# Kernel optimization log

Measured on AMD Instinct MI355X. Metric: run time of the kernel, lower is better.

Reference implementation:

```python
import jax, jax.numpy as jnp
import numpy as np
from jax import lax

T, B = 256, 4096
H = 64  # lstm hidden/input size


def setup_inputs() -> dict:
    key = jax.random.key(0)
    ks = jax.random.split(key, 20)
    s = 0.1
    return {
        "x": jax.random.normal(ks[0], (T * B, 9), jnp.float32),
        "done": jax.random.randint(ks[1], (T * B,), 0, 2).astype(jnp.int32),
        "h0": jax.random.normal(ks[2], (1, B, H), jnp.float32),
        "c0": jax.random.normal(ks[3], (1, B, H), jnp.float32),
        # root MLP: Linear(9,32) ReLU Linear(32,64) ReLU (stored [in,out])
        "Wr1": jax.random.normal(ks[4], (9, 32), jnp.float32) * s,
        "br1": jnp.zeros((32,), jnp.float32),
        "Wr2": jax.random.normal(ks[5], (32, H), jnp.float32) * s,
        "br2": jnp.zeros((H,), jnp.float32),
        # LSTM(64,64): gate order i,f,g,o; stored [in, 4H]
        "Wih": jax.random.normal(ks[6], (H, 4 * H), jnp.float32) * s,
        "Whh": jax.random.normal(ks[7], (H, 4 * H), jnp.float32) * s,
        "b_lstm": jnp.zeros((4 * H,), jnp.float32),  # bias_ih + bias_hh (both init 0)
        # critic: Linear(64,16) Tanh Linear(16,8) Tanh Linear(8,1)
        "Wc1": jax.random.normal(ks[8], (H, 16), jnp.float32) * s,
        "bc1": jnp.zeros((16,), jnp.float32),
        "Wc2": jax.random.normal(ks[9], (16, 8), jnp.float32) * s,
        "bc2": jnp.zeros((8,), jnp.float32),
        "Wc3": jax.random.normal(ks[10], (8, 1), jnp.float32) * s,
        "bc3": jnp.zeros((1,), jnp.float32),
    }


def reference(x, done, h0, c0, Wr1, br1, Wr2, br2, Wih, Whh, b_lstm,
              Wc1, bc1, Wc2, bc2, Wc3, bc3):
    b = h0.shape[1]
    # root MLP on all T*B rows at once
    hidden = jax.nn.relu(jax.nn.relu(x @ Wr1 + br1) @ Wr2 + br2)  # [T*B, 64]
    t = hidden.shape[0] // b
    hid = hidden.reshape(t, b, H)
    d = done.reshape(t, b).astype(hidden.dtype)
    # precompute input projection for all timesteps (hoisted out of the scan)
    xp = hid @ Wih + b_lstm  # [T, B, 4H]

    def step(carry, inp):
        h, c = carry
        xpt, dt = inp
        m = (1.0 - dt)[:, None]  # reset state where episode is done
        h = h * m
        c = c * m
        g = xpt + h @ Whh  # [B, 4H]
        gi, gf, gg, go = jnp.split(g, 4, axis=-1)
        c = jax.nn.sigmoid(gf) * c + jax.nn.sigmoid(gi) * jnp.tanh(gg)
        h = jax.nn.sigmoid(go) * jnp.tanh(c)
        return (h, c), h

    (_, _), hs = lax.scan(step, (h0[0], c0[0]), (xp, d))
    new_hidden = hs.reshape(t * b, H)  # flatten like torch.cat + flatten(0,1)
    # critic head (get_value)
    v = jnp.tanh(new_hidden @ Wc1 + bc1)
    v = jnp.tanh(v @ Wc2 + bc2)
    return v @ Wc3 + bc3  # [T*B, 1]
```

## Files before the change

kernel.cpp:

```cpp
#include <hip/hip_runtime.h>
#include <hip/hip_bf16.h>


#define TT 256
#define BB 4096
#define TBROWS (TT * BB)
#define LOG2E 1.44269504088896340736f

typedef short bf16x8 __attribute__((ext_vector_type(8)));
typedef float f32x4 __attribute__((ext_vector_type(4)));

__device__ __forceinline__ unsigned bfbits(float x) {
  unsigned u = __float_as_uint(x);
  return (u + 0x7fffu + ((u >> 16) & 1u)) >> 16;
}
__device__ __forceinline__ unsigned pkbf(float lo, float hi) {
  return bfbits(lo) | (bfbits(hi) << 16);
}
__device__ __forceinline__ unsigned short cvt1bf(float x) {
  unsigned pk;
  asm("v_cvt_pk_bf16_f32 %0, %1, %2" : "=v"(pk) : "v"(x), "v"(x));
  return (unsigned short)pk;
}
__device__ __forceinline__ float rcpf_(float x) { return __builtin_amdgcn_rcpf(x); }
__device__ __forceinline__ float exp2f_(float x) { return __builtin_amdgcn_exp2f(x); }

#define BAR_LDS()                                                   \
  do {                                                              \
    asm volatile("s_waitcnt lgkmcnt(0)" ::: "memory");              \
    __builtin_amdgcn_s_barrier();                                   \
    asm volatile("" ::: "memory");                                  \
  } while (0)

__global__ __launch_bounds__(256) void k1m(const float* __restrict__ x,
                                           const float* __restrict__ Wr1,
                                           const float* __restrict__ br1,
                                           const float* __restrict__ Wr2,
                                           const float* __restrict__ br2,
                                           unsigned short* __restrict__ hb) {
  __shared__ int sBr1[2 * 256];
  __shared__ int sBr2[4 * 256];
  __shared__ float sx[4][208];
  __shared__ int h1s[4][324];

  const int tid = threadIdx.x;
  const int lane = tid & 63, wid = tid >> 6;
  const int g4 = lane >> 4, l15 = lane & 15;

  for (int i = tid; i < 512; i += 256) {
    int nt = i >> 8, rem = i & 255;
    int L = rem >> 2, d = rem & 3;
    int u = nt * 16 + (L & 15);
    int k0 = (L >> 4) * 4 + d;
    float v0 = (k0 < 9) ? Wr1[k0 * 32 + u] : 0.f;
    sBr1[i] = (int)bfbits(v0);
  }
  for (int i = tid; i < 1024; i += 256) {
    int nt = i >> 8, rem = i & 255;
    int L = rem >> 2, d = rem & 3;
    int u = nt * 16 + (L & 15);
    int p = (L >> 4) * 4 + d;
    sBr2[i] = (int)pkbf(Wr2[p * 64 + u], Wr2[(p + 16) * 64 + u]);
  }
  __syncthreads();

  float br1v[2] = {br1[l15], br1[16 + l15]};
  float br2v[4];
#pragma unroll
  for (int nt = 0; nt < 4; ++nt) br2v[nt] = br2[nt * 16 + l15];

  long gw = (long)blockIdx.x * 4 + wid;
  long nw = (long)gridDim.x * 4;
  for (long row0 = gw * 16; row0 < TBROWS; row0 += nw * 16) {
    {
      int j = lane;
      float v = x[row0 * 9 + j];
      int r = (j * 456) >> 12; int cc = j - r * 9;
      sx[wid][r * 12 + cc] = v;
      j = lane + 64;
      v = x[row0 * 9 + j];
      r = (j * 456) >> 12; cc = j - r * 9;
      sx[wid][r * 12 + cc] = v;
      if (lane < 16) {
        j = lane + 128;
        v = x[row0 * 9 + j];
        r = (j * 456) >> 12; cc = j - r * 9;
        sx[wid][r * 12 + cc] = v;
      }
    }
    float4 xq = *(const float4*)&sx[wid][l15 * 12 + g4 * 4];
    union { unsigned u[4]; bf16x8 v; } A1;
#pragma unroll
    for (int d = 0; d < 4; ++d) {
      float v = ((const float*)&xq)[d];
      v = (g4 * 4 + d < 9) ? v : 0.f;
      A1.u[d] = bfbits(v);
    }
    f32x4 c1[2];
#pragma unroll
    for (int nt = 0; nt < 2; ++nt) {
      c1[nt] = (f32x4){br1v[nt], br1v[nt], br1v[nt], br1v[nt]};
      c1[nt] = __builtin_amdgcn_mfma_f32_16x16x32_bf16(
          A1.v, *(const bf16x8*)&sBr1[nt * 256 + lane * 4], c1[nt], 0, 0, 0);
    }
#pragma unroll
    for (int r = 0; r < 4; ++r)
      h1s[wid][(g4 * 4 + r) * 20 + l15] =
          (int)pkbf(fmaxf(c1[0][r], 0.f), fmaxf(c1[1][r], 0.f));
    bf16x8 A2 = *(const bf16x8*)&h1s[wid][l15 * 20 + g4 * 4];
    f32x4 c2[4];
#pragma unroll
    for (int nt = 0; nt < 4; ++nt) {
      c2[nt] = (f32x4){br2v[nt], br2v[nt], br2v[nt], br2v[nt]};
      c2[nt] = __builtin_amdgcn_mfma_f32_16x16x32_bf16(
          A2, *(const bf16x8*)&sBr2[nt * 256 + lane * 4], c2[nt], 0, 0, 0);
    }
#pragma unroll
    for (int nt = 0; nt < 4; ++nt)
#pragma unroll
      for (int r = 0; r < 4; ++r)
        hb[(row0 + g4 * 4 + r) * 64 + nt * 16 + l15] =
            (unsigned short)bfbits(fmaxf(c2[nt][r], 0.f));
  }
}

__global__ __launch_bounds__(320) void k2m(
    const unsigned short* __restrict__ hb, const int* __restrict__ done,
    const float* __restrict__ h0, const float* __restrict__ c0,
    const float* __restrict__ Wih, const float* __restrict__ Whh,
    const float* __restrict__ bl,
    const float* __restrict__ Wc1, const float* __restrict__ bc1,
    const float* __restrict__ Wc2, const float* __restrict__ bc2,
    const float* __restrict__ Wc3, const float* __restrict__ bc3,
    float* __restrict__ out) {
  __shared__ __align__(16) unsigned short hT2[2][16 * 72];
  __shared__ float sv1[16 * 20];
  __shared__ __align__(16) float smask[TT * 16];
  __shared__ int sdn[TT * 16];

  const int tid = threadIdx.x;
  const int lane = tid & 63;
  const int wid = tid >> 6;
  const int g4 = lane >> 4, l15 = lane & 15;
  const int base_b = blockIdx.x * 16;

  for (int i = tid; i < TT * 16; i += 320) {
    int d = done[(long)(i >> 4) * BB + base_b + (i & 15)];
    sdn[i] = d;
    smask[i] = 1.f - (float)d;
  }

  union frag { unsigned u[4]; bf16x8 v; };
  frag Bih[4][2], Bhh[4][2];
  frag Bc1[2];
  float wc2a[16], wc2b[16];
  float c[4];
  f32x4 bias_acc[4];
  float bc1s = 0.f, bc2s0 = 0.f, bc2s1 = 0.f, wc3a = 0.f, wc3b = 0.f, bc3r = 0.f;

  if (wid < 4) {
#pragma unroll
    for (int g = 0; g < 4; ++g) {
      int nt = g * 4 + wid;
      int col = nt * 16 + l15;
      float sc = (g == 2) ? 2.f * LOG2E : LOG2E;
#pragma unroll
      for (int q = 0; q < 2; ++q)
#pragma unroll
        for (int d = 0; d < 4; ++d) {
          int k0 = q * 32 + g4 * 8 + 2 * d;
          Bih[g][q].u[d] = pkbf(Wih[k0 * 256 + col] * sc, Wih[(k0 + 1) * 256 + col] * sc);
          Bhh[g][q].u[d] = pkbf(Whh[k0 * 256 + col] * sc, Whh[(k0 + 1) * 256 + col] * sc);
        }
      float bv = bl[nt * 16 + l15] * sc;
      bias_acc[g] = (f32x4){bv, bv, bv, bv};
    }
#pragma unroll
    for (int r = 0; r < 4; ++r) {
      int row = base_b + g4 * 4 + r;
      float m0 = 1.f - (float)done[row];
      c[r] = c0[row * 64 + wid * 16 + l15] * m0;
      hT2[1][(g4 * 4 + r) * 72 + wid * 16 + l15] =
          (unsigned short)bfbits(h0[row * 64 + wid * 16 + l15]);
    }
  } else {
    float S = 2.f * LOG2E;
#pragma unroll
    for (int q = 0; q < 2; ++q)
#pragma unroll
      for (int d = 0; d < 4; ++d) {
        int k0 = q * 32 + g4 * 8 + 2 * d;
        Bc1[q].u[d] = pkbf(Wc1[k0 * 16 + l15] * S, Wc1[(k0 + 1) * 16 + l15] * S);
      }
#pragma unroll
    for (int k = 0; k < 16; ++k) {
      wc2a[k] = Wc2[k * 8 + g4 * 2] * S;
      wc2b[k] = Wc2[k * 8 + g4 * 2 + 1] * S;
    }
    bc1s = bc1[l15] * S;
    bc2s0 = bc2[g4 * 2] * S;
    bc2s1 = bc2[g4 * 2 + 1] * S;
    wc3a = Wc3[g4 * 2];
    wc3b = Wc3[g4 * 2 + 1];
    bc3r = bc3[0];
  }
  __syncthreads();

  bf16x8 aA0 = {}, aA1 = {}, aB0 = {}, aB1 = {};
  int dnA = 0, dnB = 0;
  if (wid < 4) {
    long r0a = ((long)0 * BB + base_b + l15) * 64;
    long r1a = ((long)1 * BB + base_b + l15) * 64;
    aA0 = *(const bf16x8*)(hb + r0a + g4 * 8);
    aA1 = *(const bf16x8*)(hb + r0a + 32 + g4 * 8);
    aB0 = *(const bf16x8*)(hb + r1a + g4 * 8);
    aB1 = *(const bf16x8*)(hb + r1a + 32 + g4 * 8);
    dnA = sdn[0 * 16 + l15];
    dnB = sdn[1 * 16 + l15];
  }

  auto gate_step = [&](int t, bf16x8& x0, bf16x8& x1, int& dnv) {
    const unsigned short* rb = hT2[(t + 1) & 1];
    unsigned short* wb = hT2[t & 1];
    __builtin_amdgcn_s_setprio(1);
    int4 r0 = *(const int4*)(rb + l15 * 72 + g4 * 8);
    int4 r1 = *(const int4*)(rb + l15 * 72 + 32 + g4 * 8);
    int tm = (t + 1 < TT) ? t + 1 : t;
    float4 mn4 = *(const float4*)&smask[tm * 16 + g4 * 4];
    f32x4 acc[4];
#pragma unroll
    for (int g = 0; g < 4; ++g)
      acc[g] = __builtin_amdgcn_mfma_f32_16x16x32_bf16(x0, Bih[g][0].v, bias_acc[g], 0, 0, 0);
#pragma unroll
    for (int g = 0; g < 4; ++g)
      acc[g] = __builtin_amdgcn_mfma_f32_16x16x32_bf16(x1, Bih[g][1].v, acc[g], 0, 0, 0);
    if (dnv != 0) { r0 = make_int4(0, 0, 0, 0); r1 = make_int4(0, 0, 0, 0); }
    union { int4 i4; bf16x8 v; } ah0, ah1;
    ah0.i4 = r0; ah1.i4 = r1;
#pragma unroll
    for (int g = 0; g < 4; ++g)
      acc[g] = __builtin_amdgcn_mfma_f32_16x16x32_bf16(ah0.v, Bhh[g][0].v, acc[g], 0, 0, 0);
#pragma unroll
    for (int g = 0; g < 4; ++g)
      acc[g] = __builtin_amdgcn_mfma_f32_16x16x32_bf16(ah1.v, Bhh[g][1].v, acc[g], 0, 0, 0);
    if (t + 2 < TT) {
      long nb = ((long)(t + 2) * BB + base_b + l15) * 64;
      x0 = *(const bf16x8*)(hb + nb + g4 * 8);
      x1 = *(const bf16x8*)(hb + nb + 32 + g4 * 8);
      dnv = sdn[(t + 2) * 16 + l15];
    }
#pragma unroll
    for (int r = 0; r < 4; ++r) {
      float xi = acc[0][r], xf = acc[1][r], xg = acc[2][r], xo = acc[3][r];
      float si = rcpf_(1.f + exp2f_(-xi));
      float sf = rcpf_(1.f + exp2f_(-xf));
      float so = rcpf_(1.f + exp2f_(-xo));
      float tg = fmaf(2.f, rcpf_(1.f + exp2f_(-xg)), -1.f);
      float cc = fmaf(sf, c[r], si * tg);
      float tc = fmaf(2.f, rcpf_(1.f + exp2f_(cc * (-2.f * LOG2E))), -1.f);
      float oh = so * tc;
      c[r] = cc * ((const float*)&mn4)[r];
      wb[(g4 * 4 + r) * 72 + wid * 16 + l15] = cvt1bf(oh);
    }
    __builtin_amdgcn_s_setprio(0);
  };

  auto critic_step = [&](int tprev, const unsigned short* rb) {
    bf16x8 ca0 = *(const bf16x8*)(rb + l15 * 72 + g4 * 8);
    bf16x8 ca1 = *(const bf16x8*)(rb + l15 * 72 + 32 + g4 * 8);
    f32x4 a1 = (f32x4){bc1s, bc1s, bc1s, bc1s};
    a1 = __builtin_amdgcn_mfma_f32_16x16x32_bf16(ca0, Bc1[0].v, a1, 0, 0, 0);
    a1 = __builtin_amdgcn_mfma_f32_16x16x32_bf16(ca1, Bc1[1].v, a1, 0, 0, 0);
#pragma unroll
    for (int r = 0; r < 4; ++r) {
      float v1 = fmaf(2.f, rcpf_(1.f + exp2f_(-a1[r])), -1.f);
      sv1[(g4 * 4 + r) * 20 + l15] = v1;
    }
    float a2a = bc2s0, a2b = bc2s1;
    const float* vrow = &sv1[l15 * 20];
#pragma unroll
    for (int k = 0; k < 16; ++k) {
      float vk = vrow[k];
      a2a = fmaf(vk, wc2a[k], a2a);
      a2b = fmaf(vk, wc2b[k], a2b);
    }
    float v2a = fmaf(2.f, rcpf_(1.f + exp2f_(-a2a)), -1.f);
    float v2b = fmaf(2.f, rcpf_(1.f + exp2f_(-a2b)), -1.f);
    float p = fmaf(v2a, wc3a, v2b * wc3b);
    p += __shfl_xor(p, 16);
    p += __shfl_xor(p, 32);
    if (g4 == 0) out[(long)tprev * BB + base_b + l15] = p + bc3r;
  };

  for (int t2 = 0; t2 < TT; t2 += 2) {
    if (wid < 4) {
      gate_step(t2, aA0, aA1, dnA);
    } else {
      if (t2 > 0) critic_step(t2 - 1, hT2[(t2 + 1) & 1]);
    }
    BAR_LDS();
    if (wid < 4) {
      gate_step(t2 + 1, aB0, aB1, dnB);
    } else {
      critic_step(t2, hT2[(t2 + 2) & 1]);
    }
    BAR_LDS();
  }
  if (wid == 4) critic_step(TT - 1, hT2[(TT - 1) & 1]);
}

extern "C" void kernel_launch(void* const* d_in, const int* in_sizes, int n_in,
                              void* d_out, int out_size, void* d_ws, size_t ws_size,
                              hipStream_t stream) {
  const float* x = (const float*)d_in[0];
  const int* done = (const int*)d_in[1];
  const float* h0 = (const float*)d_in[2];
  const float* c0 = (const float*)d_in[3];
  const float* Wr1 = (const float*)d_in[4];
  const float* br1 = (const float*)d_in[5];
  const float* Wr2 = (const float*)d_in[6];
  const float* br2 = (const float*)d_in[7];
  const float* Wih = (const float*)d_in[8];
  const float* Whh = (const float*)d_in[9];
  const float* bl = (const float*)d_in[10];
  const float* Wc1 = (const float*)d_in[11];
  const float* bc1 = (const float*)d_in[12];
  const float* Wc2 = (const float*)d_in[13];
  const float* bc2 = (const float*)d_in[14];
  const float* Wc3 = (const float*)d_in[15];
  const float* bc3 = (const float*)d_in[16];
  float* out = (float*)d_out;

  unsigned short* hb = (unsigned short*)d_ws;

  k1m<<<dim3(1024), dim3(256), 0, stream>>>(x, Wr1, br1, Wr2, br2, hb);
  k2m<<<dim3(256), dim3(320), 0, stream>>>(hb, done, h0, c0, Wih, Whh, bl,
                                           Wc1, bc1, Wc2, bc2, Wc3, bc3, out);
}
```

Measured before the change: 197.5 us.

## Precompute next step's input projection off the recurrent critical path

```diff
diff --git a/kernel.cpp b/kernel.cpp
--- a/kernel.cpp
+++ b/kernel.cpp
@@ -206,20 +206,29 @@
   }
   __syncthreads();
 
+  f32x4 accP[4], accQ[4];
   bf16x8 aA0 = {}, aA1 = {}, aB0 = {}, aB1 = {};
   int dnA = 0, dnB = 0;
   if (wid < 4) {
-    long r0a = ((long)0 * BB + base_b + l15) * 64;
+    long rx = ((long)base_b + l15) * 64;
+    bf16x8 x00 = *(const bf16x8*)(hb + rx + g4 * 8);
+    bf16x8 x01 = *(const bf16x8*)(hb + rx + 32 + g4 * 8);
+#pragma unroll
+    for (int g = 0; g < 4; ++g) {
+      accP[g] = __builtin_amdgcn_mfma_f32_16x16x32_bf16(x00, Bih[g][0].v, bias_acc[g], 0, 0, 0);
+      accP[g] = __builtin_amdgcn_mfma_f32_16x16x32_bf16(x01, Bih[g][1].v, accP[g], 0, 0, 0);
+    }
     long r1a = ((long)1 * BB + base_b + l15) * 64;
-    aA0 = *(const bf16x8*)(hb + r0a + g4 * 8);
-    aA1 = *(const bf16x8*)(hb + r0a + 32 + g4 * 8);
-    aB0 = *(const bf16x8*)(hb + r1a + g4 * 8);
-    aB1 = *(const bf16x8*)(hb + r1a + 32 + g4 * 8);
+    long r2a = ((long)2 * BB + base_b + l15) * 64;
+    aA0 = *(const bf16x8*)(hb + r1a + g4 * 8);
+    aA1 = *(const bf16x8*)(hb + r1a + 32 + g4 * 8);
+    aB0 = *(const bf16x8*)(hb + r2a + g4 * 8);
+    aB1 = *(const bf16x8*)(hb + r2a + 32 + g4 * 8);
     dnA = sdn[0 * 16 + l15];
     dnB = sdn[1 * 16 + l15];
   }
 
-  auto gate_step = [&](int t, bf16x8& x0, bf16x8& x1, int& dnv) {
+  auto gate_step = [&](int t, f32x4* accW, f32x4* accN, bf16x8& x0, bf16x8& x1, int& dnv) {
     const unsigned short* rb = hT2[(t + 1) & 1];
     unsigned short* wb = hT2[t & 1];
     __builtin_amdgcn_s_setprio(1);
@@ -227,28 +236,30 @@
     int4 r1 = *(const int4*)(rb + l15 * 72 + 32 + g4 * 8);
     int tm = (t + 1 < TT) ? t + 1 : t;
     float4 mn4 = *(const float4*)&smask[tm * 16 + g4 * 4];
-    f32x4 acc[4];
-#pragma unroll
-    for (int g = 0; g < 4; ++g)
-      acc[g] = __builtin_amdgcn_mfma_f32_16x16x32_bf16(x0, Bih[g][0].v, bias_acc[g], 0, 0, 0);
-#pragma unroll
-    for (int g = 0; g < 4; ++g)
-      acc[g] = __builtin_amdgcn_mfma_f32_16x16x32_bf16(x1, Bih[g][1].v, acc[g], 0, 0, 0);
     if (dnv != 0) { r0 = make_int4(0, 0, 0, 0); r1 = make_int4(0, 0, 0, 0); }
     union { int4 i4; bf16x8 v; } ah0, ah1;
     ah0.i4 = r0; ah1.i4 = r1;
+    f32x4 acc[4];
 #pragma unroll
     for (int g = 0; g < 4; ++g)
-      acc[g] = __builtin_amdgcn_mfma_f32_16x16x32_bf16(ah0.v, Bhh[g][0].v, acc[g], 0, 0, 0);
+      acc[g] = __builtin_amdgcn_mfma_f32_16x16x32_bf16(ah0.v, Bhh[g][0].v, accW[g], 0, 0, 0);
 #pragma unroll
     for (int g = 0; g < 4; ++g)
       acc[g] = __builtin_amdgcn_mfma_f32_16x16x32_bf16(ah1.v, Bhh[g][1].v, acc[g], 0, 0, 0);
-    if (t + 2 < TT) {
-      long nb = ((long)(t + 2) * BB + base_b + l15) * 64;
+    if (t + 1 < TT) {
+#pragma unroll
+      for (int g = 0; g < 4; ++g)
+        accN[g] = __builtin_amdgcn_mfma_f32_16x16x32_bf16(x0, Bih[g][0].v, bias_acc[g], 0, 0, 0);
+#pragma unroll
+      for (int g = 0; g < 4; ++g)
+        accN[g] = __builtin_amdgcn_mfma_f32_16x16x32_bf16(x1, Bih[g][1].v, accN[g], 0, 0, 0);
+    }
+    if (t + 3 < TT) {
+      long nb = ((long)(t + 3) * BB + base_b + l15) * 64;
       x0 = *(const bf16x8*)(hb + nb + g4 * 8);
       x1 = *(const bf16x8*)(hb + nb + 32 + g4 * 8);
-      dnv = sdn[(t + 2) * 16 + l15];
-    }
+    }
+    if (t + 2 < TT) dnv = sdn[(t + 2) * 16 + l15];
 #pragma unroll
     for (int r = 0; r < 4; ++r) {
       float xi = acc[0][r], xf = acc[1][r], xg = acc[2][r], xo = acc[3][r];
@@ -294,13 +305,13 @@
 
   for (int t2 = 0; t2 < TT; t2 += 2) {
     if (wid < 4) {
-      gate_step(t2, aA0, aA1, dnA);
+      gate_step(t2, accP, accQ, aA0, aA1, dnA);
     } else {
       if (t2 > 0) critic_step(t2 - 1, hT2[(t2 + 1) & 1]);
     }
     BAR_LDS();
     if (wid < 4) {
-      gate_step(t2 + 1, aB0, aB1, dnB);
+      gate_step(t2 + 1, accQ, accP, aB0, aB1, dnB);
     } else {
       critic_step(t2, hT2[(t2 + 2) & 1]);
     }
```

Result: no change. 198.1 us, median of 3 (+0.4%).
